# Kernel optimization log

Measured on AMD Instinct MI355X. Metric: run time of the kernel, lower is better.

The kernel has to match this reference:

```python
import jax, jax.numpy as jnp
import numpy as np

L, B, T, D, H, F = 6, 4, 1024, 512, 8, 2048
DH = D // H
BIAS_DIM = 2
E = 65536
EPS = 1e-3  # LayerNormalization default epsilon in the source


def _ln(x, scale, bias):
    m = jnp.mean(x, axis=-1, keepdims=True)
    v = jnp.mean(jnp.square(x - m), axis=-1, keepdims=True)  # tf.nn.moments: population variance
    return (x - m) * jax.lax.rsqrt(v + EPS) * scale + bias


def setup_inputs() -> dict:
    key = jax.random.key(0)
    ks = jax.random.split(key, 24)
    g = lambda k, shape: (jax.random.normal(k, shape, jnp.float32) * (shape[-1] ** -0.5))
    states = jax.random.normal(ks[0], (B, T, D), jnp.float32)
    # causal mask broadcast over heads: [B, 1, Tq, Tk]
    masks = jnp.tril(jnp.ones((T, T), jnp.float32))[None, None] * jnp.ones((B, 1, 1, 1), jnp.float32)
    # sparse bias edges: columns (edge_type, batch_idx, key_idx, query_idx)
    et = jax.random.randint(ks[1], (E, 1), 0, BIAS_DIM)
    bi = jax.random.randint(ks[2], (E, 1), 0, B)
    ki = jax.random.randint(ks[3], (E, 1), 0, T)
    qi = jax.random.randint(ks[4], (E, 1), 0, T)
    attention_bias = jnp.concatenate([et, bi, ki, qi], axis=1).astype(jnp.int32)
    return dict(
        states=states,
        masks=masks,
        attention_bias=attention_bias,
        Wq=g(ks[5], (L, D, H, DH)),
        Wk=g(ks[6], (L, D, H, DH)),
        Wv=g(ks[7], (L, D, H, DH)),
        Wo=g(ks[8], (L, H, DH, D)),
        Eb=g(ks[9], (L, BIAS_DIM, DH)),
        Es=g(ks[10], (L, DH)),
        ln1_s=jnp.ones((L, D), jnp.float32),
        ln1_b=jnp.zeros((L, D), jnp.float32),
        ln2_s=jnp.ones((L, D), jnp.float32),
        ln2_b=jnp.zeros((L, D), jnp.float32),
        lno_s=jnp.ones((D,), jnp.float32),
        lno_b=jnp.zeros((D,), jnp.float32),
        W1=g(ks[11], (L, D, F)),
        b1=jnp.zeros((L, F), jnp.float32),
        W2=g(ks[12], (L, F, D)),
        b2=jnp.zeros((L, D), jnp.float32),
    )


def reference(states, masks, attention_bias, Wq, Wk, Wv, Wo, Eb, Es,
              ln1_s, ln1_b, ln2_s, ln2_b, lno_s, lno_b, W1, b1, W2, b2):
    FMIN = jnp.finfo(jnp.float32).min
    scale = jnp.float32(DH) ** -0.5
    et, bi, ki, qi = (attention_bias[:, 0], attention_bias[:, 1],
                      attention_bias[:, 2], attention_bias[:, 3])
    for l in range(L):
        # --- self-attention with edge bias ---
        x = _ln(states, ln1_s[l], ln1_b[l])
        q = jnp.einsum('btd,dha->btha', x, Wq[l])
        k = jnp.einsum('btd,dha->btha', x, Wk[l])
        v = jnp.einsum('btd,dha->btha', x, Wv[l])
        alpha = jnp.einsum('bkha,bqha->bhqk', k, q)
        # edge-type embedding -> scalar per edge, scatter into dense [B,q,k] (duplicates sum)
        bias_val = Eb[l][et] @ Es[l]  # [E]
        bias3 = jnp.zeros((B, T, T), jnp.float32).at[bi, ki, qi].add(bias_val)
        alpha = alpha + jnp.einsum('bqk,bkh->bhqk', bias3, k.sum(-1))
        alpha = alpha * scale
        alpha = alpha * masks + (1.0 - jnp.ceil(masks)) * FMIN
        alpha = jax.nn.softmax(alpha, axis=-1) * masks  # mask-softmax-renormalize (no renorm, just re-mask)
        ctx = jnp.einsum('bhqk,bkha->bqha', alpha, v)
        states = states + jnp.einsum('btha,had->btd', ctx, Wo[l])
        # --- FFN ---
        h = jax.nn.relu(_ln(states, ln2_s[l], ln2_b[l]) @ W1[l] + b1[l])
        states = states + h @ W2[l] + b2[l]
    return _ln(states, lno_s, lno_b)
```

## Files before the change

### kernel.cpp

```cpp
#include <hip/hip_runtime.h>
#include <hip/hip_bf16.h>
#include <cstdint>

#define LNUM 6
#define BNUM 4
#define TSEQ 1024
#define DMOD 512
#define HNUM 8
#define FDIM 2048
#define DHEAD 64
#define NEVENTS 65536
#define EPS_LN 1e-3f
#define ATT_SCALE 0.125f

#define GF_ACC 1
#define GF_RELU 2
#define GF_BIAS 4
#define GF_SPLIT 8
#define GF_QKV 16
#define GF_PART 32

typedef float f32x4 __attribute__((ext_vector_type(4)));
typedef short bf16x8 __attribute__((ext_vector_type(8)));
typedef unsigned short u16;
typedef unsigned int u32;

__device__ inline u16 f2bf(float f){
  u32 u = __builtin_bit_cast(u32, f);
  u32 r = (u + 0x7fffu + ((u >> 16) & 1u)) >> 16;
  return (u16)r;
}
__device__ inline float bf2f(u16 u){
  return __builtin_bit_cast(float, (u32)u << 16);
}
__device__ inline void split2(float x, u16 &hi, u16 &lo){
  u16 h = f2bf(x);
  lo = f2bf(x - bf2f(h));
  hi = h;
}
__device__ inline void gload16(const void* g, void* l){
  __builtin_amdgcn_global_load_lds(
      (const __attribute__((address_space(1))) void*)g,
      (__attribute__((address_space(3))) void*)l, 16, 0, 0);
}

__global__ __launch_bounds__(256) void ln_kernel(const float* __restrict__ x,
    const float* __restrict__ s, const float* __restrict__ bsh,
    float* __restrict__ yf, u16* __restrict__ yh, u16* __restrict__ yl, int mode){
  int row = blockIdx.x, tid = threadIdx.x;
  const float* xr = x + (size_t)row * DMOD;
  float2 v = *reinterpret_cast<const float2*>(xr + tid*2);
  float sum = v.x + v.y, sq = v.x*v.x + v.y*v.y;
  #pragma unroll
  for (int off = 32; off > 0; off >>= 1){
    sum += __shfl_down(sum, off);
    sq  += __shfl_down(sq, off);
  }
  __shared__ float ss[4], sq2[4];
  int wid = tid >> 6;
  if ((tid & 63) == 0){ ss[wid] = sum; sq2[wid] = sq; }
  __syncthreads();
  sum = ss[0]+ss[1]+ss[2]+ss[3];
  sq  = sq2[0]+sq2[1]+sq2[2]+sq2[3];
  float mean = sum * (1.f/DMOD);
  float var  = sq * (1.f/DMOD) - mean*mean;
  float rstd = rsqrtf(var + EPS_LN);
  float2 sc = *reinterpret_cast<const float2*>(s + tid*2);
  float2 bi = *reinterpret_cast<const float2*>(bsh + tid*2);
  float ox = (v.x - mean)*rstd*sc.x + bi.x;
  float oy = (v.y - mean)*rstd*sc.y + bi.y;
  if (mode == 0){
    u16 h0,l0,h1,l1;
    split2(ox,h0,l0); split2(oy,h1,l1);
    *(u32*)(yh + (size_t)row*DMOD + tid*2) = (u32)h0 | ((u32)h1<<16);
    *(u32*)(yl + (size_t)row*DMOD + tid*2) = (u32)l0 | ((u32)l1<<16);
  } else {
    float2 o; o.x = ox; o.y = oy;
    *reinterpret_cast<float2*>(yf + (size_t)row*DMOD + tid*2) = o;
  }
}

__global__ __launch_bounds__(256) void wsplit5(
    const float* __restrict__ Wq, const float* __restrict__ Wk,
    const float* __restrict__ Wv, const float* __restrict__ Wo,
    const float* __restrict__ W1, int l,
    u16* __restrict__ wqkvh, u16* __restrict__ wqkvl,
    u16* __restrict__ woh,   u16* __restrict__ wol,
    u16* __restrict__ w1h,   u16* __restrict__ w1l){
  __shared__ float T[64][65];
  int id = blockIdx.x;
  const float* src; u16 *dh, *dl; int N, bx, by;
  if (id < 256){
    const int which = id >> 6, sub = id & 63;
    bx = sub & 7; by = sub >> 3; N = 512;
    if (which == 0){ src = Wq; dh = wqkvh;            dl = wqkvl; }
    else if (which == 1){ src = Wk; dh = wqkvh + 512*512; dl = wqkvl + 512*512; }
    else if (which == 2){ src = Wv; dh = wqkvh + 2*512*512; dl = wqkvl + 2*512*512; }
    else { src = Wo; dh = woh; dl = wol; }
    src += (size_t)l*DMOD*DMOD;
  } else {
    id -= 256;
    bx = id & 31; by = id >> 5; N = 2048;
    src = W1 + (size_t)l*DMOD*FDIM; dh = w1h; dl = w1l;
  }
  const int k0 = by*64, n0 = bx*64;
  const int tid = threadIdx.x;
  {
    const int r = tid>>2, cseg = (tid&3)*16;
    const float* sp = src + (size_t)(k0+r)*N + n0 + cseg;
    #pragma unroll
    for (int i = 0; i < 16; i += 4){
      float4 v = *(const float4*)(sp + i);
      T[cseg+i+0][r] = v.x; T[cseg+i+1][r] = v.y;
      T[cseg+i+2][r] = v.z; T[cseg+i+3][r] = v.w;
    }
  }
  __syncthreads();
  const int n = tid>>2, kseg = (tid&3)*16;
  u32 wh[8], wl[8];
  #pragma unroll
  for (int i = 0; i < 8; ++i){
    u16 h0,l0,h1,l1;
    split2(T[n][kseg+2*i], h0, l0);
    split2(T[n][kseg+2*i+1], h1, l1);
    wh[i] = (u32)h0 | ((u32)h1<<16);
    wl[i] = (u32)l0 | ((u32)l1<<16);
  }
  u16* ph = dh + (size_t)(n0+n)*DMOD + k0 + kseg;
  u16* pl = dl + (size_t)(n0+n)*DMOD + k0 + kseg;
  *(uint4*)(ph)   = make_uint4(wh[0],wh[1],wh[2],wh[3]);
  *(uint4*)(ph+8) = make_uint4(wh[4],wh[5],wh[6],wh[7]);
  *(uint4*)(pl)   = make_uint4(wl[0],wl[1],wl[2],wl[3]);
  *(uint4*)(pl+8) = make_uint4(wl[4],wl[5],wl[6],wl[7]);
}

__global__ __launch_bounds__(256) void wsplit(const float* __restrict__ W,
    u16* __restrict__ Thi, u16* __restrict__ Tlo, int K, int N){
  __shared__ float T[64][65];
  const int k0 = blockIdx.y*64, n0 = blockIdx.x*64;
  const int tid = threadIdx.x;
  {
    const int r = tid>>2, cseg = (tid&3)*16;
    const float* src = W + (size_t)(k0+r)*N + n0 + cseg;
    #pragma unroll
    for (int i = 0; i < 16; i += 4){
      float4 v = *(const float4*)(src + i);
      T[cseg+i+0][r] = v.x; T[cseg+i+1][r] = v.y;
      T[cseg+i+2][r] = v.z; T[cseg+i+3][r] = v.w;
    }
  }
  __syncthreads();
  const int n = tid>>2, kseg = (tid&3)*16;
  u32 wh[8], wl[8];
  #pragma unroll
  for (int i = 0; i < 8; ++i){
    u16 h0,l0,h1,l1;
    split2(T[n][kseg+2*i], h0, l0);
    split2(T[n][kseg+2*i+1], h1, l1);
    wh[i] = (u32)h0 | ((u32)h1<<16);
    wl[i] = (u32)l0 | ((u32)l1<<16);
  }
  u16* dh = Thi + (size_t)(n0+n)*K + k0 + kseg;
  u16* dl = Tlo + (size_t)(n0+n)*K + k0 + kseg;
  *(uint4*)(dh)   = make_uint4(wh[0],wh[1],wh[2],wh[3]);
  *(uint4*)(dh+8) = make_uint4(wh[4],wh[5],wh[6],wh[7]);
  *(uint4*)(dl)   = make_uint4(wl[0],wl[1],wl[2],wl[3]);
  *(uint4*)(dl+8) = make_uint4(wl[4],wl[5],wl[6],wl[7]);
}

template<int BN, int NS, int FLAGS>
__global__ __launch_bounds__(256) void gemm_mfma(
    const u16* __restrict__ Ahi, const u16* __restrict__ Alo,
    const u16* __restrict__ Bhi, const u16* __restrict__ Blo,
    const float* __restrict__ bias, float* __restrict__ C,
    u16* __restrict__ Ohi, u16* __restrict__ Olo,
    u16* __restrict__ Vhi, u16* __restrict__ Vlo,
    int M, int N, int K, int kc){
  constexpr int NA  = 16;
  constexpr int NB  = BN/8;
  constexpr int PER = (NA+NB)/4;
  __shared__ __align__(16) unsigned char As[128*128];
  __shared__ __align__(16) unsigned char Bs[BN*128];
  const int tid = threadIdx.x, wid = tid>>6, lane = tid&63;
  const int li = lane&15, g = lane>>4;
  const int nxb = N/BN;
  const int cpx = gridDim.x >> 3;
  const int bid = blockIdx.x;
  const int wg  = (bid&7)*cpx + (bid>>3);
  const int bx = wg % nxb, by = wg / nxb;
  const int m0 = by*128, n0 = bx*BN;
  const int wr = wid>>1, wc = wid&1;
  const int kbeg = blockIdx.y * kc, kend = kbeg + kc;
  f32x4 acc[4][NS] = {};

  for (int k0 = kbeg; k0 < kend; k0 += 32){
    __syncthreads();
    #pragma unroll
    for (int i = 0; i < PER; ++i){
      const int issue = wid*PER + i;
      const bool isA = issue < NA;
      const int ia = isA ? issue : issue - NA;
      const int c = ia*64 + lane;
      const int row = c>>3, slot = c&7;
      const int sg = slot ^ (row&7);
      const u16* base = isA ? (sg < 4 ? Ahi : Alo) : (sg < 4 ? Bhi : Blo);
      const int gr = (isA ? m0 : n0) + row;
      const u16* gp = base + (size_t)gr*K + k0 + (sg&3)*8;
      unsigned char* lp = (isA ? As : Bs) + ia*1024 + lane*16;
      gload16(gp, lp);
    }
    __syncthreads();
    bf16x8 ah[4], al[4], bh[NS], bl[NS];
    #pragma unroll
    for (int ms = 0; ms < 4; ++ms){
      const int r = wr*64 + ms*16 + li; const int x = (r&7)<<4;
      const unsigned char* p = As + r*128;
      ah[ms] = *(const bf16x8*)(p + ((g*16)^x));
      al[ms] = *(const bf16x8*)(p + ((64 + g*16)^x));
    }
    #pragma unroll
    for (int ns = 0; ns < NS; ++ns){
      const int r = wc*(BN/2) + ns*16 + li; const int x = (r&7)<<4;
      const unsigned char* p = Bs + r*128;
      bh[ns] = *(const bf16x8*)(p + ((g*16)^x));
      bl[ns] = *(const bf16x8*)(p + ((64 + g*16)^x));
    }
    #pragma unroll
    for (int ms = 0; ms < 4; ++ms)
      #pragma unroll
      for (int ns = 0; ns < NS; ++ns){
        acc[ms][ns] = __builtin_amdgcn_mfma_f32_16x16x32_bf16(ah[ms], bh[ns], acc[ms][ns], 0, 0, 0);
        acc[ms][ns] = __builtin_amdgcn_mfma_f32_16x16x32_bf16(ah[ms], bl[ns], acc[ms][ns], 0, 0, 0);
        acc[ms][ns] = __builtin_amdgcn_mfma_f32_16x16x32_bf16(al[ms], bh[ns], acc[ms][ns], 0, 0, 0);
      }
  }
  #pragma unroll
  for (int ms = 0; ms < 4; ++ms){
    #pragma unroll
    for (int ns = 0; ns < NS; ++ns){
      #pragma unroll
      for (int r = 0; r < 4; ++r){
        const int m = m0 + wr*64 + ms*16 + g*4 + r;
        const int n = n0 + wc*(BN/2) + ns*16 + li;
        float val = acc[ms][ns][r];
        if (FLAGS & GF_BIAS) val += bias[n];
        if (FLAGS & GF_RELU) val = fmaxf(val, 0.f);
        if (FLAGS & GF_QKV){
          u16 vh, vl; split2(val, vh, vl);
          if (n < 1024){
            const size_t ix = (size_t)m*1024 + n;
            Ohi[ix] = vh; Olo[ix] = vl;
          } else {
            const size_t ix = ((size_t)(m>>10)*DMOD + (n-1024))*TSEQ + (m&1023);
            Vhi[ix] = vh; Vlo[ix] = vl;
          }
        } else if (FLAGS & GF_SPLIT){
          u16 vh, vl; split2(val, vh, vl);
          const size_t ix = (size_t)m*N + n;
          Ohi[ix] = vh; Olo[ix] = vl;
        } else if (FLAGS & GF_PART){
          C[(size_t)blockIdx.y*M*N + (size_t)m*N + n] = val;
        } else {
          const size_t ix = (size_t)m*N + n;
          if (FLAGS & GF_ACC) val += C[ix];
          C[ix] = val;
        }
      }
    }
  }
}

__global__ __launch_bounds__(256) void red2(const float* __restrict__ part,
    const float* __restrict__ bias, float* __restrict__ states, int hasb){
  const size_t MN = (size_t)BNUM*TSEQ*DMOD;
  const size_t i4 = ((size_t)blockIdx.x*256 + threadIdx.x)*4;
  float4 a = *(const float4*)(part + i4);
  float4 b = *(const float4*)(part + MN + i4);
  float4 s = *(const float4*)(states + i4);
  s.x += a.x + b.x;
  s.y += a.y + b.y;
  s.z += a.z + b.z;
  s.w += a.w + b.w;
  if (hasb){
    float4 bb = *(const float4*)(bias + (int)(i4 & (DMOD-1)));
    s.x += bb.x; s.y += bb.y; s.z += bb.z; s.w += bb.w;
  }
  *(float4*)(states + i4) = s;
}

__global__ __launch_bounds__(256) void ksum_kernel(const u16* __restrict__ kh_,
    const u16* __restrict__ kl_, float* __restrict__ ks){
  int idx = blockIdx.x*256 + threadIdx.x;
  const size_t base = (size_t)(idx>>3)*1024 + 512 + (idx&7)*DHEAD;
  const u16* ph = kh_ + base;
  const u16* pl = kl_ + base;
  float s = 0.f;
  #pragma unroll
  for (int a = 0; a < DHEAD; a += 8){
    bf16x8 vh = *(const bf16x8*)(ph + a);
    bf16x8 vl = *(const bf16x8*)(pl + a);
    #pragma unroll
    for (int j = 0; j < 8; ++j) s += bf2f((u16)vh[j]) + bf2f((u16)vl[j]);
  }
  ks[idx] = s;
}

__global__ __launch_bounds__(256) void scatter_kernel(const int* __restrict__ ab,
    const float* __restrict__ Eb, const float* __restrict__ Es, float* __restrict__ bias3){
  int e = blockIdx.x*256 + threadIdx.x;
  if (e >= NEVENTS) return;
  int4 r = *reinterpret_cast<const int4*>(ab + (size_t)e*4);
  const float* eb = Eb + (size_t)r.x * DHEAD;
  float val = 0.f;
  #pragma unroll
  for (int a = 0; a < DHEAD; ++a) val += eb[a]*Es[a];
  atomicAdd(bias3 + ((size_t)r.y*TSEQ + r.z)*TSEQ + r.w, val);
}

__global__ __launch_bounds__(256) void attn_split(
    const u16* __restrict__ qkh, const u16* __restrict__ qkl,
    const u16* __restrict__ vth, const u16* __restrict__ vtl,
    const float* __restrict__ ksum, const float* __restrict__ bias3,
    u16* __restrict__ ch_, u16* __restrict__ cl_){
  __shared__ __align__(16) unsigned char Klh[8192], Kll[8192];
  __shared__ __align__(16) unsigned char Vh[8192], Vl[8192];
  __shared__ __align__(16) unsigned char Plh[8192], Pll[8192];
  __shared__ float ksl[64];

  const int bid = blockIdx.x;
  const int qb = bid & 15, h = (bid >> 4) & 7, b = bid >> 7;
  const int q0 = qb * 64;
  const int tid = threadIdx.x, wid = tid >> 6, lane = tid & 63;
  const int li = lane & 15, g = lane >> 4;
  const int rowg0 = q0 + wid*16 + g*4;

  bf16x8 qah[2], qal[2];
  {
    const int qrow = q0 + wid*16 + li;
    const size_t qoff = (size_t)(b*TSEQ + qrow)*1024 + h*DHEAD;
    #pragma unroll
    for (int k2 = 0; k2 < 2; ++k2){
      qah[k2] = *(const bf16x8*)(qkh + qoff + g*8 + k2*32);
      qal[k2] = *(const bf16x8*)(qkl + qoff + g*8 + k2*32);
    }
  }

  f32x4 oacc[4] = {};
  float mrun[4] = {-INFINITY, -INFINITY, -INFINITY, -INFINITY};
  float srun[4] = {0.f, 0.f, 0.f, 0.f};

  for (int kt = 0; kt <= q0; kt += 64){
    __syncthreads();
    {
      const int krow = tid >> 2, part = tid & 3;
      const int base = krow*128, x = (krow & 7) << 4;
      const size_t koff = (size_t)(b*TSEQ + kt + krow)*1024 + 512 + h*DHEAD + part*16;
      uint4 a0 = *(const uint4*)(qkh + koff);
      uint4 a1 = *(const uint4*)(qkh + koff + 8);
      uint4 a2 = *(const uint4*)(qkl + koff);
      uint4 a3 = *(const uint4*)(qkl + koff + 8);
      *(uint4*)(Klh + base + ((part*32     )^x)) = a0;
      *(uint4*)(Klh + base + ((part*32 + 16)^x)) = a1;
      *(uint4*)(Kll + base + ((part*32     )^x)) = a2;
      *(uint4*)(Kll + base + ((part*32 + 16)^x)) = a3;
      const size_t voff = ((size_t)b*DMOD + h*DHEAD + krow)*TSEQ + kt + part*16;
      uint4 v0 = *(const uint4*)(vth + voff);
      uint4 v1 = *(const uint4*)(vth + voff + 8);
      uint4 v2 = *(const uint4*)(vtl + voff);
      uint4 v3 = *(const uint4*)(vtl + voff + 8);
      *(uint4*)(Vh + base + ((part*32     )^x)) = v0;
      *(uint4*)(Vh + base + ((part*32 + 16)^x)) = v1;
      *(uint4*)(Vl + base + ((part*32     )^x)) = v2;
      *(uint4*)(Vl + base + ((part*32 + 16)^x)) = v3;
    }
    if (tid < 64) ksl[tid] = ksum[(size_t)(b*TSEQ + kt + tid)*HNUM + h];
    __syncthreads();

    f32x4 sacc[4] = {};
    #pragma unroll
    for (int jb = 0; jb < 4; ++jb){
      const int rb = (jb*16 + li)*128, x = (li & 7) << 4;
      #pragma unroll
      for (int k2 = 0; k2 < 2; ++k2){
        bf16x8 kfh = *(const bf16x8*)(Klh + rb + ((g*16 + k2*64)^x));
        bf16x8 kfl = *(const bf16x8*)(Kll + rb + ((g*16 + k2*64)^x));
        sacc[jb] = __builtin_amdgcn_mfma_f32_16x16x32_bf16(qah[k2], kfh, sacc[jb], 0, 0, 0);
        sacc[jb] = __builtin_amdgcn_mfma_f32_16x16x32_bf16(qah[k2], kfl, sacc[jb], 0, 0, 0);
        sacc[jb] = __builtin_amdgcn_mfma_f32_16x16x32_bf16(qal[k2], kfh, sacc[jb], 0, 0, 0);
      }
    }
    const float* bb = bias3 + (size_t)b*TSEQ*TSEQ;
    #pragma unroll
    for (int jb = 0; jb < 4; ++jb){
      const int colg = kt + jb*16 + li;
      const float ksv = ksl[jb*16 + li];
      #pragma unroll
      for (int r = 0; r < 4; ++r){
        const int rowg = rowg0 + r;
        float s = (sacc[jb][r] + bb[(size_t)rowg*TSEQ + colg] * ksv) * ATT_SCALE;
        sacc[jb][r] = (colg <= rowg) ? s : -INFINITY;
      }
    }
    #pragma unroll
    for (int r = 0; r < 4; ++r){
      float tm = fmaxf(fmaxf(sacc[0][r], sacc[1][r]), fmaxf(sacc[2][r], sacc[3][r]));
      tm = fmaxf(tm, __shfl_xor(tm, 1));
      tm = fmaxf(tm, __shfl_xor(tm, 2));
      tm = fmaxf(tm, __shfl_xor(tm, 4));
      tm = fmaxf(tm, __shfl_xor(tm, 8));
      const float nm = fmaxf(mrun[r], tm);
      const float fac = __expf(mrun[r] - nm);
      mrun[r] = nm;
      float p0 = __expf(sacc[0][r] - nm);
      float p1 = __expf(sacc[1][r] - nm);
      float p2 = __expf(sacc[2][r] - nm);
      float p3 = __expf(sacc[3][r] - nm);
      float rs = p0 + p1 + p2 + p3;
      rs += __shfl_xor(rs, 1);
      rs += __shfl_xor(rs, 2);
      rs += __shfl_xor(rs, 4);
      rs += __shfl_xor(rs, 8);
      srun[r] = srun[r]*fac + rs;
      oacc[0][r] *= fac; oacc[1][r] *= fac; oacc[2][r] *= fac; oacc[3][r] *= fac;
      const int prow = g*4 + r;
      const int pb = wid*2048 + prow*128, px = (prow & 7) << 4;
      u16 ph0,pl0, ph1,pl1, ph2,pl2, ph3,pl3;
      split2(p0,ph0,pl0); split2(p1,ph1,pl1); split2(p2,ph2,pl2); split2(p3,ph3,pl3);
      *(u16*)(Plh + pb + ((li*2 +  0)^px)) = ph0;
      *(u16*)(Plh + pb + ((li*2 + 32)^px)) = ph1;
      *(u16*)(Plh + pb + ((li*2 + 64)^px)) = ph2;
      *(u16*)(Plh + pb + ((li*2 + 96)^px)) = ph3;
      *(u16*)(Pll + pb + ((li*2 +  0)^px)) = pl0;
      *(u16*)(Pll + pb + ((li*2 + 32)^px)) = pl1;
      *(u16*)(Pll + pb + ((li*2 + 64)^px)) = pl2;
      *(u16*)(Pll + pb + ((li*2 + 96)^px)) = pl3;
    }
    bf16x8 pah[2], pal[2];
    {
      const int pb = wid*2048 + li*128, x = (li & 7) << 4;
      pah[0] = *(const bf16x8*)(Plh + pb + ((g*16     )^x));
      pah[1] = *(const bf16x8*)(Plh + pb + ((g*16 + 64)^x));
      pal[0] = *(const bf16x8*)(Pll + pb + ((g*16     )^x));
      pal[1] = *(const bf16x8*)(Pll + pb + ((g*16 + 64)^x));
    }
    #pragma unroll
    for (int ja = 0; ja < 4; ++ja){
      const int vb = (ja*16 + li)*128, x = (li & 7) << 4;
      #pragma unroll
      for (int k2 = 0; k2 < 2; ++k2){
        bf16x8 vfh = *(const bf16x8*)(Vh + vb + ((g*16 + k2*64)^x));
        bf16x8 vfl = *(const bf16x8*)(Vl + vb + ((g*16 + k2*64)^x));
        oacc[ja] = __builtin_amdgcn_mfma_f32_16x16x32_bf16(pah[k2], vfh, oacc[ja], 0, 0, 0);
        oacc[ja] = __builtin_amdgcn_mfma_f32_16x16x32_bf16(pah[k2], vfl, oacc[ja], 0, 0, 0);
        oacc[ja] = __builtin_amdgcn_mfma_f32_16x16x32_bf16(pal[k2], vfh, oacc[ja], 0, 0, 0);
      }
    }
  }

  #pragma unroll
  for (int ja = 0; ja < 4; ++ja){
    #pragma unroll
    for (int r = 0; r < 4; ++r){
      const int rowg = rowg0 + r;
      const float val = oacc[ja][r] / srun[r];
      u16 vh, vl; split2(val, vh, vl);
      const size_t ix = (size_t)(b*TSEQ + rowg)*DMOD + h*DHEAD + ja*16 + li;
      ch_[ix] = vh; cl_[ix] = vl;
    }
  }
}

extern "C" void kernel_launch(void* const* d_in, const int* in_sizes, int n_in,
                              void* d_out, int out_size, void* d_ws, size_t ws_size,
                              hipStream_t stream){
  const float* states0 = (const float*)d_in[0];
  const int*   ab      = (const int*)d_in[2];
  const float* Wq = (const float*)d_in[3];
  const float* Wk = (const float*)d_in[4];
  const float* Wv = (const float*)d_in[5];
  const float* Wo = (const float*)d_in[6];
  const float* Eb = (const float*)d_in[7];
  const float* Es = (const float*)d_in[8];
  const float* ln1_s = (const float*)d_in[9];
  const float* ln1_b = (const float*)d_in[10];
  const float* ln2_s = (const float*)d_in[11];
  const float* ln2_b = (const float*)d_in[12];
  const float* lno_s = (const float*)d_in[13];
  const float* lno_b = (const float*)d_in[14];
  const float* W1 = (const float*)d_in[15];
  const float* b1 = (const float*)d_in[16];
  const float* W2 = (const float*)d_in[17];
  const float* b2 = (const float*)d_in[18];
  float* out = (float*)d_out;

  char* ws = (char*)d_ws;
  const size_t MB = 1024*1024;
  float* states = (float*)(ws);
  u16* xh  = (u16*)(ws + 8*MB);
  u16* xl  = (u16*)(ws + 12*MB);
  u16* qkh = (u16*)(ws + 16*MB);
  u16* qkl = (u16*)(ws + 24*MB);
  u16* vth = (u16*)(ws + 32*MB);
  u16* vtl = (u16*)(ws + 36*MB);
  u16* cth = (u16*)(ws + 40*MB);
  u16* ctl = (u16*)(ws + 44*MB);
  float* ksum  = (float*)(ws + 48*MB);
  float* bias3 = (float*)(ws + 48*MB + 131072);
  char*  wA    = ws + 64*MB + 131072;
  char*  wB    = wA + 4*MB;
  u16* hh = qkh;
  u16* hl = vth;
  float* part = bias3;

  u16* wqkvh = (u16*)(wA);
  u16* wqkvl = (u16*)(wA + 1536*1024);
  u16* woh   = (u16*)(wA + 3*MB);
  u16* wol   = (u16*)(wA + 3*MB + 512*1024);
  u16* w2h   = (u16*)(wA);
  u16* w2l   = (u16*)(wA + 2*MB);
  u16* w1h   = (u16*)(wB);
  u16* w1l   = (u16*)(wB + 2*MB);

  hipMemcpyAsync(states, states0, 8*MB, hipMemcpyDeviceToDevice, stream);

  const int NROW = BNUM*TSEQ;
  dim3 blk(256);
  for (int l = 0; l < LNUM; ++l){
    wsplit5<<<512, blk, 0, stream>>>(Wq, Wk, Wv, Wo, W1, l,
        wqkvh, wqkvl, woh, wol, w1h, w1l);

    ln_kernel<<<NROW, blk, 0, stream>>>(states, ln1_s + l*DMOD, ln1_b + l*DMOD, nullptr, xh, xl, 0);
    gemm_mfma<128,4, GF_SPLIT|GF_QKV><<<384, blk, 0, stream>>>(
        xh, xl, wqkvh, wqkvl, nullptr, nullptr, qkh, qkl, vth, vtl, NROW, 1536, DMOD, DMOD);
    ksum_kernel<<<(BNUM*TSEQ*HNUM)/256, blk, 0, stream>>>(qkh, qkl, ksum);
    hipMemsetAsync(bias3, 0, (size_t)BNUM*TSEQ*TSEQ*sizeof(float), stream);
    scatter_kernel<<<NEVENTS/256, blk, 0, stream>>>(ab, Eb + (size_t)l*2*DHEAD, Es + (size_t)l*DHEAD, bias3);
    attn_split<<<BNUM*HNUM*(TSEQ/64), blk, 0, stream>>>(qkh, qkl, vth, vtl, ksum, bias3, cth, ctl);
    gemm_mfma<64,2, GF_PART><<<dim3(256,2), blk, 0, stream>>>(
        cth, ctl, woh, wol, nullptr, part, nullptr, nullptr, nullptr, nullptr, NROW, DMOD, DMOD, DMOD/2);
    red2<<<(NROW*DMOD)/1024, blk, 0, stream>>>(part, b2, states, 0);

    wsplit<<<dim3(8,32), blk, 0, stream>>>(W2 + (size_t)l*FDIM*DMOD, w2h, w2l, FDIM, DMOD);
    ln_kernel<<<NROW, blk, 0, stream>>>(states, ln2_s + l*DMOD, ln2_b + l*DMOD, nullptr, xh, xl, 0);
    gemm_mfma<128,4, GF_BIAS|GF_RELU|GF_SPLIT><<<512, blk, 0, stream>>>(
        xh, xl, w1h, w1l, b1 + (size_t)l*FDIM, nullptr, hh, hl, nullptr, nullptr, NROW, FDIM, DMOD, DMOD);
    gemm_mfma<64,2, GF_PART><<<dim3(256,2), blk, 0, stream>>>(
        hh, hl, w2h, w2l, nullptr, part, nullptr, nullptr, nullptr, nullptr, NROW, DMOD, FDIM, FDIM/2);
    red2<<<(NROW*DMOD)/1024, blk, 0, stream>>>(part, b2 + (size_t)l*DMOD, states, 1);
  }
  ln_kernel<<<NROW, blk, 0, stream>>>(states, lno_s, lno_b, out, nullptr, nullptr, 1);
}
```

Baseline: 1.368 ms.

## Pair causal query blocks per workgroup and prefetch K/V tiles in attention

The attention kernel now gives each workgroup two query blocks, p and 15-p, so every block does the same amount of causal work, and the grid shrinks from 512 to 256 blocks. The K/V tiles loaded into shared memory serve both query blocks, and the next tile's global loads go into registers while the current tile is computed. The scatter kernel now computes the two edge-type bias scalars once per block instead of a 64-term dot product per edge. The trade-offs are fewer blocks to fill the GPU, more register pressure from two sets of accumulators, and a dropped bounds check that only holds because the edge count divides evenly by 256.

Result: faster. 1.314 ms (-3.9%).

```diff
diff --git a/kernel.cpp b/kernel.cpp
--- a/kernel.cpp
+++ b/kernel.cpp
@@ -307,14 +307,105 @@
 
 __global__ __launch_bounds__(256) void scatter_kernel(const int* __restrict__ ab,
     const float* __restrict__ Eb, const float* __restrict__ Es, float* __restrict__ bias3){
+  __shared__ float d2[2];
+  if (threadIdx.x < 2){
+    float v = 0.f;
+    #pragma unroll
+    for (int a = 0; a < DHEAD; ++a) v += Eb[threadIdx.x*DHEAD + a]*Es[a];
+    d2[threadIdx.x] = v;
+  }
+  __syncthreads();
   int e = blockIdx.x*256 + threadIdx.x;
-  if (e >= NEVENTS) return;
   int4 r = *reinterpret_cast<const int4*>(ab + (size_t)e*4);
-  const float* eb = Eb + (size_t)r.x * DHEAD;
-  float val = 0.f;
-  #pragma unroll
-  for (int a = 0; a < DHEAD; ++a) val += eb[a]*Es[a];
-  atomicAdd(bias3 + ((size_t)r.y*TSEQ + r.z)*TSEQ + r.w, val);
+  atomicAdd(bias3 + ((size_t)r.y*TSEQ + r.z)*TSEQ + r.w, d2[r.x]);
+}
+
+__device__ __forceinline__ void tile_compute(
+    const unsigned char* __restrict__ Klh, const unsigned char* __restrict__ Kll,
+    const unsigned char* __restrict__ Vh, const unsigned char* __restrict__ Vl,
+    unsigned char* __restrict__ Plh, unsigned char* __restrict__ Pll,
+    const float* __restrict__ ksl, const float* __restrict__ bb,
+    int kt, int rowg0, int wid, int li, int g,
+    const bf16x8* qah, const bf16x8* qal,
+    f32x4* oacc, float* mrun, float* srun){
+  f32x4 sacc[4] = {};
+  #pragma unroll
+  for (int jb = 0; jb < 4; ++jb){
+    const int rb = (jb*16 + li)*128, x = (li & 7) << 4;
+    #pragma unroll
+    for (int k2 = 0; k2 < 2; ++k2){
+      bf16x8 kfh = *(const bf16x8*)(Klh + rb + ((g*16 + k2*64)^x));
+      bf16x8 kfl = *(const bf16x8*)(Kll + rb + ((g*16 + k2*64)^x));
+      sacc[jb] = __builtin_amdgcn_mfma_f32_16x16x32_bf16(qah[k2], kfh, sacc[jb], 0, 0, 0);
+      sacc[jb] = __builtin_amdgcn_mfma_f32_16x16x32_bf16(qah[k2], kfl, sacc[jb], 0, 0, 0);
+      sacc[jb] = __builtin_amdgcn_mfma_f32_16x16x32_bf16(qal[k2], kfh, sacc[jb], 0, 0, 0);
+    }
+  }
+  #pragma unroll
+  for (int jb = 0; jb < 4; ++jb){
+    const int colg = kt + jb*16 + li;
+    const float ksv = ksl[jb*16 + li];
+    #pragma unroll
+    for (int r = 0; r < 4; ++r){
+      const int rowg = rowg0 + r;
+      float s = (sacc[jb][r] + bb[(size_t)rowg*TSEQ + colg] * ksv) * ATT_SCALE;
+      sacc[jb][r] = (colg <= rowg) ? s : -INFINITY;
+    }
+  }
+  #pragma unroll
+  for (int r = 0; r < 4; ++r){
+    float tm = fmaxf(fmaxf(sacc[0][r], sacc[1][r]), fmaxf(sacc[2][r], sacc[3][r]));
+    tm = fmaxf(tm, __shfl_xor(tm, 1));
+    tm = fmaxf(tm, __shfl_xor(tm, 2));
+    tm = fmaxf(tm, __shfl_xor(tm, 4));
+    tm = fmaxf(tm, __shfl_xor(tm, 8));
+    const float nm = fmaxf(mrun[r], tm);
+    const float fac = __expf(mrun[r] - nm);
+    mrun[r] = nm;
+    float p0 = __expf(sacc[0][r] - nm);
+    float p1 = __expf(sacc[1][r] - nm);
+    float p2 = __expf(sacc[2][r] - nm);
+    float p3 = __expf(sacc[3][r] - nm);
+    float rs = p0 + p1 + p2 + p3;
+    rs += __shfl_xor(rs, 1);
+    rs += __shfl_xor(rs, 2);
+    rs += __shfl_xor(rs, 4);
+    rs += __shfl_xor(rs, 8);
+    srun[r] = srun[r]*fac + rs;
+    oacc[0][r] *= fac; oacc[1][r] *= fac; oacc[2][r] *= fac; oacc[3][r] *= fac;
+    const int prow = g*4 + r;
+    const int pb = wid*2048 + prow*128, px = (prow & 7) << 4;
+    u16 ph0,pl0, ph1,pl1, ph2,pl2, ph3,pl3;
+    split2(p0,ph0,pl0); split2(p1,ph1,pl1); split2(p2,ph2,pl2); split2(p3,ph3,pl3);
+    *(u16*)(Plh + pb + ((li*2 +  0)^px)) = ph0;
+    *(u16*)(Plh + pb + ((li*2 + 32)^px)) = ph1;
+    *(u16*)(Plh + pb + ((li*2 + 64)^px)) = ph2;
+    *(u16*)(Plh + pb + ((li*2 + 96)^px)) = ph3;
+    *(u16*)(Pll + pb + ((li*2 +  0)^px)) = pl0;
+    *(u16*)(Pll + pb + ((li*2 + 32)^px)) = pl1;
+    *(u16*)(Pll + pb + ((li*2 + 64)^px)) = pl2;
+    *(u16*)(Pll + pb + ((li*2 + 96)^px)) = pl3;
+  }
+  bf16x8 pah[2], pal[2];
+  {
+    const int pb = wid*2048 + li*128, x = (li & 7) << 4;
+    pah[0] = *(const bf16x8*)(Plh + pb + ((g*16     )^x));
+    pah[1] = *(const bf16x8*)(Plh + pb + ((g*16 + 64)^x));
+    pal[0] = *(const bf16x8*)(Pll + pb + ((g*16     )^x));
+    pal[1] = *(const bf16x8*)(Pll + pb + ((g*16 + 64)^x));
+  }
+  #pragma unroll
+  for (int ja = 0; ja < 4; ++ja){
+    const int vb = (ja*16 + li)*128, x = (li & 7) << 4;
+    #pragma unroll
+    for (int k2 = 0; k2 < 2; ++k2){
+      bf16x8 vfh = *(const bf16x8*)(Vh + vb + ((g*16 + k2*64)^x));
+      bf16x8 vfl = *(const bf16x8*)(Vl + vb + ((g*16 + k2*64)^x));
+      oacc[ja] = __builtin_amdgcn_mfma_f32_16x16x32_bf16(pah[k2], vfh, oacc[ja], 0, 0, 0);
+      oacc[ja] = __builtin_amdgcn_mfma_f32_16x16x32_bf16(pah[k2], vfl, oacc[ja], 0, 0, 0);
+      oacc[ja] = __builtin_amdgcn_mfma_f32_16x16x32_bf16(pal[k2], vfh, oacc[ja], 0, 0, 0);
+    }
+  }
 }
 
 __global__ __launch_bounds__(256) void attn_split(
@@ -322,150 +413,94 @@
     const u16* __restrict__ vth, const u16* __restrict__ vtl,
     const float* __restrict__ ksum, const float* __restrict__ bias3,
     u16* __restrict__ ch_, u16* __restrict__ cl_){
-  __shared__ __align__(16) unsigned char Klh[8192], Kll[8192];
-  __shared__ __align__(16) unsigned char Vh[8192], Vl[8192];
+  __shared__ __align__(16) unsigned char Klh[8192], Kll[8192], Vh[8192], Vl[8192];
   __shared__ __align__(16) unsigned char Plh[8192], Pll[8192];
   __shared__ float ksl[64];
 
   const int bid = blockIdx.x;
-  const int qb = bid & 15, h = (bid >> 4) & 7, b = bid >> 7;
-  const int q0 = qb * 64;
+  const int p = bid & 7, h = (bid >> 3) & 7, b = bid >> 6;
+  const int qA0 = p*64, qB0 = (15-p)*64;
   const int tid = threadIdx.x, wid = tid >> 6, lane = tid & 63;
   const int li = lane & 15, g = lane >> 4;
-  const int rowg0 = q0 + wid*16 + g*4;
-
-  bf16x8 qah[2], qal[2];
+  const int rowA0 = qA0 + wid*16 + g*4;
+  const int rowB0 = qB0 + wid*16 + g*4;
+
+  bf16x8 qahA[2], qalA[2], qahB[2], qalB[2];
   {
-    const int qrow = q0 + wid*16 + li;
-    const size_t qoff = (size_t)(b*TSEQ + qrow)*1024 + h*DHEAD;
+    const size_t offA = (size_t)(b*TSEQ + qA0 + wid*16 + li)*1024 + h*DHEAD;
+    const size_t offB = (size_t)(b*TSEQ + qB0 + wid*16 + li)*1024 + h*DHEAD;
     #pragma unroll
     for (int k2 = 0; k2 < 2; ++k2){
-      qah[k2] = *(const bf16x8*)(qkh + qoff + g*8 + k2*32);
-      qal[k2] = *(const bf16x8*)(qkl + qoff + g*8 + k2*32);
-    }
-  }
-
-  f32x4 oacc[4] = {};
-  float mrun[4] = {-INFINITY, -INFINITY, -INFINITY, -INFINITY};
-  float srun[4] = {0.f, 0.f, 0.f, 0.f};
-
-  for (int kt = 0; kt <= q0; kt += 64){
+      qahA[k2] = *(const bf16x8*)(qkh + offA + g*8 + k2*32);
+      qalA[k2] = *(const bf16x8*)(qkl + offA + g*8 + k2*32);
+      qahB[k2] = *(const bf16x8*)(qkh + offB + g*8 + k2*32);
+      qalB[k2] = *(const bf16x8*)(qkl + offB + g*8 + k2*32);
+    }
+  }
+
+  f32x4 oaccA[4] = {}, oaccB[4] = {};
+  float mrunA[4] = {-INFINITY,-INFINITY,-INFINITY,-INFINITY};
+  float mrunB[4] = {-INFINITY,-INFINITY,-INFINITY,-INFINITY};
+  float srunA[4] = {0.f,0.f,0.f,0.f};
+  float srunB[4] = {0.f,0.f,0.f,0.f};
+
+  const int krow = tid >> 2, part = tid & 3;
+  const int lbase = krow*128, lx = (krow & 7) << 4;
+  const float* bb = bias3 + (size_t)b*TSEQ*TSEQ;
+
+  uint4 rk0, rk1, rk2, rk3, rv0, rv1, rv2, rv3;
+  float ksr = 0.f;
+  auto issue = [&](int kt){
+    const size_t koff = (size_t)(b*TSEQ + kt + krow)*1024 + 512 + h*DHEAD + part*16;
+    rk0 = *(const uint4*)(qkh + koff);
+    rk1 = *(const uint4*)(qkh + koff + 8);
+    rk2 = *(const uint4*)(qkl + koff);
+    rk3 = *(const uint4*)(qkl + koff + 8);
+    const size_t voff = ((size_t)b*DMOD + h*DHEAD + krow)*TSEQ + kt + part*16;
+    rv0 = *(const uint4*)(vth + voff);
+    rv1 = *(const uint4*)(vth + voff + 8);
+    rv2 = *(const uint4*)(vtl + voff);
+    rv3 = *(const uint4*)(vtl + voff + 8);
+    if (tid < 64) ksr = ksum[(size_t)(b*TSEQ + kt + tid)*HNUM + h];
+  };
+
+  issue(0);
+  for (int kt = 0; kt <= qB0; kt += 64){
+    *(uint4*)(Klh + lbase + ((part*32     )^lx)) = rk0;
+    *(uint4*)(Klh + lbase + ((part*32 + 16)^lx)) = rk1;
+    *(uint4*)(Kll + lbase + ((part*32     )^lx)) = rk2;
+    *(uint4*)(Kll + lbase + ((part*32 + 16)^lx)) = rk3;
+    *(uint4*)(Vh  + lbase + ((part*32     )^lx)) = rv0;
+    *(uint4*)(Vh  + lbase + ((part*32 + 16)^lx)) = rv1;
+    *(uint4*)(Vl  + lbase + ((part*32     )^lx)) = rv2;
+    *(uint4*)(Vl  + lbase + ((part*32 + 16)^lx)) = rv3;
+    if (tid < 64) ksl[tid] = ksr;
     __syncthreads();
-    {
-      const int krow = tid >> 2, part = tid & 3;
-      const int base = krow*128, x = (krow & 7) << 4;
-      const size_t koff = (size_t)(b*TSEQ + kt + krow)*1024 + 512 + h*DHEAD + part*16;
-      uint4 a0 = *(const uint4*)(qkh + koff);
-      uint4 a1 = *(const uint4*)(qkh + koff + 8);
-      uint4 a2 = *(const uint4*)(qkl + koff);
-      uint4 a3 = *(const uint4*)(qkl + koff + 8);
-      *(uint4*)(Klh + base + ((part*32     )^x)) = a0;
-      *(uint4*)(Klh + base + ((part*32 + 16)^x)) = a1;
-      *(uint4*)(Kll + base + ((part*32     )^x)) = a2;
-      *(uint4*)(Kll + base + ((part*32 + 16)^x)) = a3;
-      const size_t voff = ((size_t)b*DMOD + h*DHEAD + krow)*TSEQ + kt + part*16;
-      uint4 v0 = *(const uint4*)(vth + voff);
-      uint4 v1 = *(const uint4*)(vth + voff + 8);
-      uint4 v2 = *(const uint4*)(vtl + voff);
-      uint4 v3 = *(const uint4*)(vtl + voff + 8);
-      *(uint4*)(Vh + base + ((part*32     )^x)) = v0;
-      *(uint4*)(Vh + base + ((part*32 + 16)^x)) = v1;
-      *(uint4*)(Vl + base + ((part*32     )^x)) = v2;
-      *(uint4*)(Vl + base + ((part*32 + 16)^x)) = v3;
-    }
-    if (tid < 64) ksl[tid] = ksum[(size_t)(b*TSEQ + kt + tid)*HNUM + h];
+    if (kt + 64 <= qB0) issue(kt + 64);
+    tile_compute(Klh, Kll, Vh, Vl, Plh, Pll, ksl, bb, kt, rowB0, wid, li, g,
+                 qahB, qalB, oaccB, mrunB, srunB);
+    if (kt <= qA0)
+      tile_compute(Klh, Kll, Vh, Vl, Plh, Pll, ksl, bb, kt, rowA0, wid, li, g,
+                   qahA, qalA, oaccA, mrunA, srunA);
     __syncthreads();
-
-    f32x4 sacc[4] = {};
-    #pragma unroll
-    for (int jb = 0; jb < 4; ++jb){
-      const int rb = (jb*16 + li)*128, x = (li & 7) << 4;
-      #pragma unroll
-      for (int k2 = 0; k2 < 2; ++k2){
-        bf16x8 kfh = *(const bf16x8*)(Klh + rb + ((g*16 + k2*64)^x));
-        bf16x8 kfl = *(const bf16x8*)(Kll + rb + ((g*16 + k2*64)^x));
-        sacc[jb] = __builtin_amdgcn_mfma_f32_16x16x32_bf16(qah[k2], kfh, sacc[jb], 0, 0, 0);
-        sacc[jb] = __builtin_amdgcn_mfma_f32_16x16x32_bf16(qah[k2], kfl, sacc[jb], 0, 0, 0);
-        sacc[jb] = __builtin_amdgcn_mfma_f32_16x16x32_bf16(qal[k2], kfh, sacc[jb], 0, 0, 0);
+  }
+
+  #pragma unroll
+  for (int ja = 0; ja < 4; ++ja){
+    #pragma unroll
+    for (int r = 0; r < 4; ++r){
+      {
+        const float val = oaccB[ja][r] / srunB[r];
+        u16 vh, vl; split2(val, vh, vl);
+        const size_t ix = (size_t)(b*TSEQ + rowB0 + r)*DMOD + h*DHEAD + ja*16 + li;
+        ch_[ix] = vh; cl_[ix] = vl;
       }
-    }
-    const float* bb = bias3 + (size_t)b*TSEQ*TSEQ;
-    #pragma unroll
-    for (int jb = 0; jb < 4; ++jb){
-      const int colg = kt + jb*16 + li;
-      const float ksv = ksl[jb*16 + li];
-      #pragma unroll
-      for (int r = 0; r < 4; ++r){
-        const int rowg = rowg0 + r;
-        float s = (sacc[jb][r] + bb[(size_t)rowg*TSEQ + colg] * ksv) * ATT_SCALE;
-        sacc[jb][r] = (colg <= rowg) ? s : -INFINITY;
+      {
+        const float val = oaccA[ja][r] / srunA[r];
+        u16 vh, vl; split2(val, vh, vl);
+        const size_t ix = (size_t)(b*TSEQ + rowA0 + r)*DMOD + h*DHEAD + ja*16 + li;
+        ch_[ix] = vh; cl_[ix] = vl;
       }
-    }
-    #pragma unroll
-    for (int r = 0; r < 4; ++r){
-      float tm = fmaxf(fmaxf(sacc[0][r], sacc[1][r]), fmaxf(sacc[2][r], sacc[3][r]));
-      tm = fmaxf(tm, __shfl_xor(tm, 1));
-      tm = fmaxf(tm, __shfl_xor(tm, 2));
-      tm = fmaxf(tm, __shfl_xor(tm, 4));
-      tm = fmaxf(tm, __shfl_xor(tm, 8));
-      const float nm = fmaxf(mrun[r], tm);
-      const float fac = __expf(mrun[r] - nm);
-      mrun[r] = nm;
-      float p0 = __expf(sacc[0][r] - nm);
-      float p1 = __expf(sacc[1][r] - nm);
-      float p2 = __expf(sacc[2][r] - nm);
-      float p3 = __expf(sacc[3][r] - nm);
-      float rs = p0 + p1 + p2 + p3;
-      rs += __shfl_xor(rs, 1);
-      rs += __shfl_xor(rs, 2);
-      rs += __shfl_xor(rs, 4);
-      rs += __shfl_xor(rs, 8);
-      srun[r] = srun[r]*fac + rs;
-      oacc[0][r] *= fac; oacc[1][r] *= fac; oacc[2][r] *= fac; oacc[3][r] *= fac;
-      const int prow = g*4 + r;
-      const int pb = wid*2048 + prow*128, px = (prow & 7) << 4;
-      u16 ph0,pl0, ph1,pl1, ph2,pl2, ph3,pl3;
-      split2(p0,ph0,pl0); split2(p1,ph1,pl1); split2(p2,ph2,pl2); split2(p3,ph3,pl3);
-      *(u16*)(Plh + pb + ((li*2 +  0)^px)) = ph0;
-      *(u16*)(Plh + pb + ((li*2 + 32)^px)) = ph1;
-      *(u16*)(Plh + pb + ((li*2 + 64)^px)) = ph2;
-      *(u16*)(Plh + pb + ((li*2 + 96)^px)) = ph3;
-      *(u16*)(Pll + pb + ((li*2 +  0)^px)) = pl0;
-      *(u16*)(Pll + pb + ((li*2 + 32)^px)) = pl1;
-      *(u16*)(Pll + pb + ((li*2 + 64)^px)) = pl2;
-      *(u16*)(Pll + pb + ((li*2 + 96)^px)) = pl3;
-    }
-    bf16x8 pah[2], pal[2];
-    {
-      const int pb = wid*2048 + li*128, x = (li & 7) << 4;
-      pah[0] = *(const bf16x8*)(Plh + pb + ((g*16     )^x));
-      pah[1] = *(const bf16x8*)(Plh + pb + ((g*16 + 64)^x));
-      pal[0] = *(const bf16x8*)(Pll + pb + ((g*16     )^x));
-      pal[1] = *(const bf16x8*)(Pll + pb + ((g*16 + 64)^x));
-    }
-    #pragma unroll
-    for (int ja = 0; ja < 4; ++ja){
-      const int vb = (ja*16 + li)*128, x = (li & 7) << 4;
-      #pragma unroll
-      for (int k2 = 0; k2 < 2; ++k2){
-        bf16x8 vfh = *(const bf16x8*)(Vh + vb + ((g*16 + k2*64)^x));
-        bf16x8 vfl = *(const bf16x8*)(Vl + vb + ((g*16 + k2*64)^x));
-        oacc[ja] = __builtin_amdgcn_mfma_f32_16x16x32_bf16(pah[k2], vfh, oacc[ja], 0, 0, 0);
-        oacc[ja] = __builtin_amdgcn_mfma_f32_16x16x32_bf16(pah[k2], vfl, oacc[ja], 0, 0, 0);
-        oacc[ja] = __builtin_amdgcn_mfma_f32_16x16x32_bf16(pal[k2], vfh, oacc[ja], 0, 0, 0);
-      }
-    }
-  }
-
-  #pragma unroll
-  for (int ja = 0; ja < 4; ++ja){
-    #pragma unroll
-    for (int r = 0; r < 4; ++r){
-      const int rowg = rowg0 + r;
-      const float val = oacc[ja][r] / srun[r];
-      u16 vh, vl; split2(val, vh, vl);
-      const size_t ix = (size_t)(b*TSEQ + rowg)*DMOD + h*DHEAD + ja*16 + li;
-      ch_[ix] = vh; cl_[ix] = vl;
     }
   }
 }
@@ -535,7 +570,7 @@
     ksum_kernel<<<(BNUM*TSEQ*HNUM)/256, blk, 0, stream>>>(qkh, qkl, ksum);
     hipMemsetAsync(bias3, 0, (size_t)BNUM*TSEQ*TSEQ*sizeof(float), stream);
     scatter_kernel<<<NEVENTS/256, blk, 0, stream>>>(ab, Eb + (size_t)l*2*DHEAD, Es + (size_t)l*DHEAD, bias3);
-    attn_split<<<BNUM*HNUM*(TSEQ/64), blk, 0, stream>>>(qkh, qkl, vth, vtl, ksum, bias3, cth, ctl);
+    attn_split<<<BNUM*HNUM*8, blk, 0, stream>>>(qkh, qkl, vth, vtl, ksum, bias3, cth, ctl);
     gemm_mfma<64,2, GF_PART><<<dim3(256,2), blk, 0, stream>>>(
         cth, ctl, woh, wol, nullptr, part, nullptr, nullptr, nullptr, nullptr, NROW, DMOD, DMOD, DMOD/2);
     red2<<<(NROW*DMOD)/1024, blk, 0, stream>>>(part, b2, states, 0);
```
